# Kernel tuning notes

Measured on AMD Instinct MI355X. Metric: run time of the kernel, lower is better.

Reference implementation:

```python
import jax, jax.numpy as jnp
import numpy as np

K_EXPERTS = 2  # init kwarg k_experts

def _glu_mlp(x, up_w, gate_w, down_w):
    # gated MLP: down( up(x) * GELU(gate(x)) ), exact-erf GELU matching torch nn.GELU()
    h = (x @ up_w) * jax.nn.gelu(x @ gate_w, approximate=False)
    return h @ down_w

def setup_inputs() -> dict:
    key = jax.random.key(0)
    ks = jax.random.split(key, 8)
    B, S, D, I, E = 2, 2048, 1024, 512, 8
    sc = 0.02
    return {
        "x": jax.random.normal(ks[0], (B, S, D), jnp.float32),
        "gate_w": jax.random.normal(ks[1], (E, D), jnp.float32) * sc,
        "up_w": jax.random.normal(ks[2], (E, D, I), jnp.float32) * sc,
        "gproj_w": jax.random.normal(ks[3], (E, D, I), jnp.float32) * sc,
        "down_w": jax.random.normal(ks[4], (E, I, D), jnp.float32) * sc,
        "shared_up_w": jax.random.normal(ks[5], (D, I), jnp.float32) * sc,
        "shared_gate_w": jax.random.normal(ks[6], (D, I), jnp.float32) * sc,
        "shared_down_w": jax.random.normal(ks[7], (I, D), jnp.float32) * sc,
    }

def reference(x, gate_w, up_w, gproj_w, down_w, shared_up_w, shared_gate_w, shared_down_w):
    B, S, D = x.shape
    E = gate_w.shape[0]
    xf = x.reshape(-1, D)                      # [T, D]
    T = xf.shape[0]

    # --- SigmaGate: softmax over expert logits, top-k, renormalize ---
    logits = xf @ gate_w.T                     # [T, E]
    scores = jax.nn.softmax(logits, axis=-1)
    topk_w, topk_idx = jax.lax.top_k(scores, K_EXPERTS)   # [T, k]
    topk_w = topk_w / (topk_w.sum(axis=-1, keepdims=True) + 1e-20)

    # combine weights as dense [T, E] (topk indices are distinct per token)
    combine = jnp.zeros((T, E), xf.dtype).at[jnp.arange(T)[:, None], topk_idx].add(topk_w)

    # --- experts: scan over E, accumulate weighted expert outputs ---
    def step(acc, ws):
        uw, gw, dw, ce = ws                    # ce: [T] combine weight for this expert
        y_e = _glu_mlp(xf, uw, gw, dw)         # [T, D]
        return acc + ce[:, None] * y_e, None

    y, _ = jax.lax.scan(step, jnp.zeros_like(xf), (up_w, gproj_w, down_w, combine.T))

    # --- shared expert on identity ---
    y = y + _glu_mlp(xf, shared_up_w, shared_gate_w, shared_down_w)
    return y.reshape(B, S, D)
```

## Files before the change

kernel.cpp:

```cpp
#include <hip/hip_runtime.h>
#include <hip/hip_bf16.h>
#include <math.h>

#define T_TOK 4096
#define D_DIM 1024
#define I_DIM 512
#define E_EXP 8
#define KSEL 2
#define NPAIR (T_TOK * KSEL)
#define ROUTED_CAP 10240
#define SHARED_BASE ROUTED_CAP
#define RTOT (ROUTED_CAP + T_TOK)
#define MAXTILES 56
#define GRID_G (MAXTILES * 4)

typedef __bf16 bf16x8 __attribute__((ext_vector_type(8)));
typedef float f32x4 __attribute__((ext_vector_type(4)));
typedef unsigned short ushort8 __attribute__((ext_vector_type(8)));

constexpr size_t SZ_XB  = (size_t)T_TOK * D_DIM * 2;
constexpr size_t SZ_UG  = (size_t)E_EXP * 2 * I_DIM * D_DIM * 2;
constexpr size_t SZ_DT  = (size_t)E_EXP * I_DIM * D_DIM * 2;
constexpr size_t SZ_SUG = (size_t)2 * I_DIM * D_DIM * 2;
constexpr size_t SZ_SDT = (size_t)I_DIM * D_DIM * 2;
constexpr size_t SZ_H   = (size_t)RTOT * I_DIM * 2;
constexpr size_t SZ_Y   = (size_t)RTOT * D_DIM * 2;

constexpr size_t OFF_XB   = 0;
constexpr size_t OFF_UG   = OFF_XB  + SZ_XB;
constexpr size_t OFF_DT   = OFF_UG  + SZ_UG;
constexpr size_t OFF_SUG  = OFF_DT  + SZ_DT;
constexpr size_t OFF_SDT  = OFF_SUG + SZ_SUG;
constexpr size_t OFF_H    = OFF_SDT + SZ_SDT;
constexpr size_t OFF_Y    = OFF_H   + SZ_H;
constexpr size_t OFF_TOPKI= OFF_Y   + SZ_Y;
constexpr size_t OFF_TOPKW= OFF_TOPKI + (size_t)NPAIR * 4;
constexpr size_t OFF_INV  = OFF_TOPKW + (size_t)NPAIR * 4;
constexpr size_t OFF_PERM = OFF_INV   + (size_t)NPAIR * 4;
constexpr size_t OFF_META = OFF_PERM  + (size_t)RTOT * 4;

__device__ __forceinline__ unsigned short f2bf(float f) {
  unsigned int u = __float_as_uint(f);
  unsigned int r = (u + 0x7FFFu + ((u >> 16) & 1u)) >> 16;
  return (unsigned short)r;
}
__device__ __forceinline__ float bf2f(unsigned short s) {
  return __uint_as_float(((unsigned int)s) << 16);
}
__device__ __forceinline__ void gload_lds16(const void* g, void* l) {
  __builtin_amdgcn_global_load_lds(
      (const __attribute__((address_space(1))) void*)g,
      (__attribute__((address_space(3))) void*)l, 16, 0, 0);
}

__global__ void transpose_cvt_all(
    const float* __restrict__ upw, const float* __restrict__ gpw,
    const float* __restrict__ dww, const float* __restrict__ sup,
    const float* __restrict__ sgt, const float* __restrict__ sdw,
    unsigned short* __restrict__ UG, unsigned short* __restrict__ sUG,
    unsigned short* __restrict__ Dt, unsigned short* __restrict__ sDt) {
  __shared__ float t[32][33];
  int bid = blockIdx.x;
  const float* in; unsigned short* out;
  int R, C, xt, yt, mode;
  if (bid < 4096)       { int e = bid >> 9, s = bid & 511;
    in = upw + (size_t)e * D_DIM * I_DIM; out = UG + (size_t)e * 2 * I_DIM * D_DIM;
    R = D_DIM; C = I_DIM; xt = s & 15; yt = s >> 4; mode = 0; }
  else if (bid < 8192)  { int b = bid - 4096; int e = b >> 9, s = b & 511;
    in = gpw + (size_t)e * D_DIM * I_DIM; out = UG + (size_t)e * 2 * I_DIM * D_DIM;
    R = D_DIM; C = I_DIM; xt = s & 15; yt = s >> 4; mode = 1; }
  else if (bid < 12288) { int b = bid - 8192; int e = b >> 9, s = b & 511;
    in = dww + (size_t)e * I_DIM * D_DIM; out = Dt + (size_t)e * I_DIM * D_DIM;
    R = I_DIM; C = D_DIM; xt = s & 31; yt = s >> 5; mode = 2; }
  else if (bid < 12800) { int s = bid - 12288;
    in = sup; out = sUG; R = D_DIM; C = I_DIM; xt = s & 15; yt = s >> 4; mode = 0; }
  else if (bid < 13312) { int s = bid - 12800;
    in = sgt; out = sUG; R = D_DIM; C = I_DIM; xt = s & 15; yt = s >> 4; mode = 1; }
  else                  { int s = bid - 13312;
    in = sdw; out = sDt; R = I_DIM; C = D_DIM; xt = s & 31; yt = s >> 5; mode = 2; }
  int c0 = xt * 32, r0 = yt * 32;
  int tx = threadIdx.x, ty = threadIdx.y;
#pragma unroll
  for (int i = 0; i < 4; ++i)
    t[ty + 8 * i][tx] = in[(size_t)(r0 + ty + 8 * i) * C + c0 + tx];
  __syncthreads();
#pragma unroll
  for (int i = 0; i < 4; ++i) {
    int c = c0 + ty + 8 * i;
    int orow = (mode == 2) ? c : (((c >> 4) << 5) + (c & 15) + (mode == 1 ? 16 : 0));
    out[(size_t)orow * R + r0 + tx] = f2bf(t[tx][ty + 8 * i]);
  }
}

__global__ void gating_kernel(const float* __restrict__ x, const float* __restrict__ gw,
                              unsigned short* __restrict__ xb,
                              int* __restrict__ topk_idx, float* __restrict__ topk_w) {
  int lane = threadIdx.x & 63;
  int t = blockIdx.x * 4 + (threadIdx.x >> 6);
  const float4* xr = (const float4*)(x + (size_t)t * D_DIM);
  float4 xv[4];
#pragma unroll
  for (int j = 0; j < 4; ++j) xv[j] = xr[lane + 64 * j];
#pragma unroll
  for (int j = 0; j < 4; ++j) {
    ushort4 o;
    o.x = f2bf(xv[j].x); o.y = f2bf(xv[j].y); o.z = f2bf(xv[j].z); o.w = f2bf(xv[j].w);
    *(ushort4*)&xb[(size_t)t * D_DIM + (lane + 64 * j) * 4] = o;
  }
  float acc[E_EXP];
#pragma unroll
  for (int e = 0; e < E_EXP; ++e) {
    const float4* gr = (const float4*)(gw + (size_t)e * D_DIM);
    float a = 0.f;
#pragma unroll
    for (int j = 0; j < 4; ++j) {
      float4 g = gr[lane + 64 * j];
      a += xv[j].x * g.x + xv[j].y * g.y + xv[j].z * g.z + xv[j].w * g.w;
    }
    acc[e] = a;
  }
#pragma unroll
  for (int off = 32; off; off >>= 1)
#pragma unroll
    for (int e = 0; e < E_EXP; ++e) acc[e] += __shfl_xor(acc[e], off, 64);
  if (lane == 0) {
    int i0 = 0; float m0 = acc[0];
#pragma unroll
    for (int e = 1; e < E_EXP; ++e) if (acc[e] > m0) { m0 = acc[e]; i0 = e; }
    int i1 = -1; float m1 = -1e30f;
#pragma unroll
    for (int e = 0; e < E_EXP; ++e) if (e != i0 && acc[e] > m1) { m1 = acc[e]; i1 = e; }
    float e1 = __expf(m1 - m0);
    float w0 = 1.0f / (1.0f + e1);
    float w1 = e1 / (1.0f + e1);
    topk_idx[2 * t] = i0; topk_idx[2 * t + 1] = i1;
    topk_w[2 * t] = w0;   topk_w[2 * t + 1] = w1;
  }
}

__global__ __launch_bounds__(1024) void route_kernel(
    const int* __restrict__ tidx, int* __restrict__ meta,
    int* __restrict__ perm, int* __restrict__ inv) {
  __shared__ int els[NPAIR];
  __shared__ int cnt_iw[128][E_EXP];
  __shared__ int base_iw[128][E_EXP];
  __shared__ int ebase[E_EXP];
  __shared__ int ecnt[E_EXP];
  int tid = threadIdx.x, lane = tid & 63, wv = tid >> 6;

  for (int it = 0; it < NPAIR / 1024; ++it) {
    int g = it * 1024 + tid;
    int e = tidx[g];
    els[g] = e;
#pragma unroll
    for (int ex = 0; ex < E_EXP; ++ex) {
      unsigned long long m = __ballot(e == ex);
      if (lane == 0) cnt_iw[it * 16 + wv][ex] = __popcll(m);
    }
  }
  __syncthreads();

  if (tid < E_EXP) {
    int s = 0;
    for (int iw = 0; iw < 128; ++iw) { base_iw[iw][tid] = s; s += cnt_iw[iw][tid]; }
    ecnt[tid] = s;
  }
  __syncthreads();

  if (tid == 0) {
    int o = 0, tc = 0;
    int2* m2 = (int2*)meta;
    for (int e = 0; e < E_EXP; ++e) {
      ebase[e] = o;
      int c = ecnt[e];
      int pt = (c + 255) >> 8;
      for (int ti = 0; ti < pt; ++ti) m2[tc++] = make_int2(e, o + ti * 256);
      o += pt * 256;
    }
    for (int ti = 0; ti < T_TOK / 256; ++ti)
      m2[tc++] = make_int2(E_EXP, SHARED_BASE + ti * 256);
    for (; tc < MAXTILES; ++tc) m2[tc] = make_int2(-1, 0);
  }
  __syncthreads();

  for (int it = 0; it < NPAIR / 1024; ++it) {
    int g = it * 1024 + tid;
    int e = els[g];
    int rank = 0;
#pragma unroll
    for (int ex = 0; ex < E_EXP; ++ex) {
      unsigned long long m = __ballot(e == ex);
      if (e == ex) rank = __popcll(m & ((1ull << lane) - 1ull));
    }
    int row = ebase[e] + base_iw[it * 16 + wv][e] + rank;
    perm[row] = g >> 1;
    inv[g] = row;
  }
  for (int p = tid; p < E_EXP * 256; p += 1024) {
    int e = p >> 8, s = p & 255;
    int c = ecnt[e];
    int padn = (((c + 255) >> 8) << 8) - c;
    if (s < padn) perm[ebase[e] + c + s] = 0;
  }
  for (int t = tid; t < T_TOK; t += 1024) perm[SHARED_BASE + t] = t;
}

__global__ __launch_bounds__(512, 2) void gemm1_kernel(
    const unsigned short* __restrict__ xb, const unsigned short* __restrict__ UG,
    const unsigned short* __restrict__ sUG, unsigned short* __restrict__ H,
    const int* __restrict__ meta, const int* __restrict__ perm) {
  int orig = blockIdx.x;
  int wg = (orig & 7) * (GRID_G / 8) + (orig >> 3);
  int mt = wg >> 2, nt = wg & 3;
  int2 m2 = ((const int2*)meta)[mt];
  int e = m2.x;
  if (e < 0) return;
  int base = m2.y;
  int n0 = nt * 256;
  const unsigned short* B = (e < E_EXP) ? UG + (size_t)e * 2 * I_DIM * D_DIM : sUG;

  __shared__ unsigned short As[2 * 256 * 64];
  __shared__ unsigned short Bs[2 * 256 * 64];

  int tid = threadIdx.x, lane = tid & 63, wv = tid >> 6;
  const unsigned short *gA[4], *gB[4];
  int dL[4];
#pragma unroll
  for (int j = 0; j < 4; ++j) {
    int c = j * 512 + tid;
    int row = c >> 3, q = c & 7, qs = q ^ (row & 7);
    int tok = perm[base + row];
    gA[j] = xb + (size_t)tok * D_DIM + qs * 8;
    gB[j] = B + (size_t)(n0 + row) * D_DIM + qs * 8;
    dL[j] = (j * 512 + wv * 64) * 8;
  }

  f32x4 acc[8][4] = {};
  int wr = (wv >> 2) * 128, wc = (wv & 3) * 64;
  int l15 = lane & 15, l4 = lane >> 4;
  int sx = l15 & 7;

#define STAGE1(buf, k0) do { \
  _Pragma("unroll") \
  for (int j = 0; j < 4; ++j) { \
    gload_lds16(gA[j] + (k0), As + (buf) * 16384 + dL[j]); \
    gload_lds16(gB[j] + (k0), Bs + (buf) * 16384 + dL[j]); \
  } } while (0)

  STAGE1(0, 0);
  const int NK = D_DIM / 64;
  for (int t = 0; t < NK; ++t) {
    int cur = t & 1;
    if (t + 1 < NK) {
      STAGE1(cur ^ 1, (t + 1) * 64);
      asm volatile("s_waitcnt vmcnt(8)" ::: "memory");
    } else {
      asm volatile("s_waitcnt vmcnt(0)" ::: "memory");
    }
    __builtin_amdgcn_s_barrier();
#pragma unroll
    for (int kh = 0; kh < 2; ++kh) {
      int kb = kh * 4 + l4;
      bf16x8 af[8], bfr[4];
#pragma unroll
      for (int i = 0; i < 8; ++i)
        af[i] = *reinterpret_cast<const bf16x8*>(&As[cur * 16384 + (wr + i * 16 + l15) * 64 + (kb ^ sx) * 8]);
#pragma unroll
      for (int j = 0; j < 4; ++j)
        bfr[j] = *reinterpret_cast<const bf16x8*>(&Bs[cur * 16384 + (wc + j * 16 + l15) * 64 + (kb ^ sx) * 8]);
      __builtin_amdgcn_s_setprio(1);
#pragma unroll
      for (int i = 0; i < 8; ++i)
#pragma unroll
        for (int j = 0; j < 4; ++j)
          acc[i][j] = __builtin_amdgcn_mfma_f32_16x16x32_bf16(af[i], bfr[j], acc[i][j], 0, 0, 0);
      __builtin_amdgcn_s_setprio(0);
    }
    asm volatile("" ::: "memory");
    __builtin_amdgcn_s_barrier();
  }
#undef STAGE1

  const float is2 = 0.70710678118654752f;
  int cb = ((n0 + wc) >> 1);
#pragma unroll
  for (int i = 0; i < 8; ++i) {
    int row = base + wr + i * 16 + l4 * 4;
#pragma unroll
    for (int p = 0; p < 2; ++p) {
      int col = cb + p * 16 + l15;
#pragma unroll
      for (int r = 0; r < 4; ++r) {
        float u = acc[i][2 * p][r], g = acc[i][2 * p + 1][r];
        float gl = 0.5f * g * (1.0f + erff(g * is2));
        H[(size_t)(row + r) * I_DIM + col] = f2bf(u * gl);
      }
    }
  }
}

__global__ __launch_bounds__(512, 2) void gemm2_kernel(
    const unsigned short* __restrict__ H, const unsigned short* __restrict__ Dt,
    const unsigned short* __restrict__ sDt, unsigned short* __restrict__ Y,
    const int* __restrict__ meta) {
  int orig = blockIdx.x;
  int wg = (orig & 7) * (GRID_G / 8) + (orig >> 3);
  int mt = wg >> 2, nt = wg & 3;
  int2 m2 = ((const int2*)meta)[mt];
  int e = m2.x;
  if (e < 0) return;
  int base = m2.y;
  int n0 = nt * 256;
  const unsigned short* B = (e < E_EXP) ? Dt + (size_t)e * D_DIM * I_DIM : sDt;

  __shared__ unsigned short As[2 * 256 * 64];
  __shared__ unsigned short Bs[2 * 256 * 64];

  int tid = threadIdx.x, lane = tid & 63, wv = tid >> 6;
  const unsigned short *gA[4], *gB[4];
  int dL[4];
#pragma unroll
  for (int j = 0; j < 4; ++j) {
    int c = j * 512 + tid;
    int row = c >> 3, q = c & 7, qs = q ^ (row & 7);
    gA[j] = H + (size_t)(base + row) * I_DIM + qs * 8;
    gB[j] = B + (size_t)(n0 + row) * I_DIM + qs * 8;
    dL[j] = (j * 512 + wv * 64) * 8;
  }

  f32x4 acc[8][4] = {};
  int wr = (wv >> 2) * 128, wc = (wv & 3) * 64;
  int l15 = lane & 15, l4 = lane >> 4;
  int sx = l15 & 7;

#define STAGE2(buf, k0) do { \
  _Pragma("unroll") \
  for (int j = 0; j < 4; ++j) { \
    gload_lds16(gA[j] + (k0), As + (buf) * 16384 + dL[j]); \
    gload_lds16(gB[j] + (k0), Bs + (buf) * 16384 + dL[j]); \
  } } while (0)

  STAGE2(0, 0);
  const int NK = I_DIM / 64;
  for (int t = 0; t < NK; ++t) {
    int cur = t & 1;
    if (t + 1 < NK) {
      STAGE2(cur ^ 1, (t + 1) * 64);
      asm volatile("s_waitcnt vmcnt(8)" ::: "memory");
    } else {
      asm volatile("s_waitcnt vmcnt(0)" ::: "memory");
    }
    __builtin_amdgcn_s_barrier();
#pragma unroll
    for (int kh = 0; kh < 2; ++kh) {
      int kb = kh * 4 + l4;
      bf16x8 af[8], bfr[4];
#pragma unroll
      for (int i = 0; i < 8; ++i)
        af[i] = *reinterpret_cast<const bf16x8*>(&As[cur * 16384 + (wr + i * 16 + l15) * 64 + (kb ^ sx) * 8]);
#pragma unroll
      for (int j = 0; j < 4; ++j)
        bfr[j] = *reinterpret_cast<const bf16x8*>(&Bs[cur * 16384 + (wc + j * 16 + l15) * 64 + (kb ^ sx) * 8]);
      __builtin_amdgcn_s_setprio(1);
#pragma unroll
      for (int i = 0; i < 8; ++i)
#pragma unroll
        for (int j = 0; j < 4; ++j)
          acc[i][j] = __builtin_amdgcn_mfma_f32_16x16x32_bf16(af[i], bfr[j], acc[i][j], 0, 0, 0);
      __builtin_amdgcn_s_setprio(0);
    }
    asm volatile("" ::: "memory");
    __builtin_amdgcn_s_barrier();
  }
#undef STAGE2

#pragma unroll
  for (int i = 0; i < 8; ++i) {
    int row = base + wr + i * 16 + l4 * 4;
#pragma unroll
    for (int j = 0; j < 4; ++j) {
      int col = n0 + wc + j * 16 + l15;
#pragma unroll
      for (int r = 0; r < 4; ++r)
        Y[(size_t)(row + r) * D_DIM + col] = f2bf(acc[i][j][r]);
    }
  }
}

__global__ void combine_kernel(const unsigned short* __restrict__ Y, const int* __restrict__ inv,
                               const float* __restrict__ tw, float* __restrict__ out) {
  int g = blockIdx.x * 256 + threadIdx.x;
  int t = g >> 7, d0 = (g & 127) * 8;
  int r0 = inv[2 * t], r1 = inv[2 * t + 1];
  float w0 = tw[2 * t], w1 = tw[2 * t + 1];
  ushort8 y0 = *(const ushort8*)&Y[(size_t)r0 * D_DIM + d0];
  ushort8 y1 = *(const ushort8*)&Y[(size_t)r1 * D_DIM + d0];
  ushort8 ys = *(const ushort8*)&Y[(size_t)(SHARED_BASE + t) * D_DIM + d0];
  float o[8];
#pragma unroll
  for (int j = 0; j < 8; ++j)
    o[j] = w0 * bf2f(y0[j]) + w1 * bf2f(y1[j]) + bf2f(ys[j]);
  float4* op = (float4*)(out + (size_t)t * D_DIM + d0);
  op[0] = make_float4(o[0], o[1], o[2], o[3]);
  op[1] = make_float4(o[4], o[5], o[6], o[7]);
}

extern "C" void kernel_launch(void* const* d_in, const int* in_sizes, int n_in,
                              void* d_out, int out_size, void* d_ws, size_t ws_size,
                              hipStream_t stream) {
  const float* x    = (const float*)d_in[0];
  const float* gw   = (const float*)d_in[1];
  const float* upw  = (const float*)d_in[2];
  const float* gpw  = (const float*)d_in[3];
  const float* dww  = (const float*)d_in[4];
  const float* sup  = (const float*)d_in[5];
  const float* sgt  = (const float*)d_in[6];
  const float* sdw  = (const float*)d_in[7];
  float* out = (float*)d_out;

  char* ws = (char*)d_ws;
  unsigned short* xb  = (unsigned short*)(ws + OFF_XB);
  unsigned short* UG  = (unsigned short*)(ws + OFF_UG);
  unsigned short* Dt  = (unsigned short*)(ws + OFF_DT);
  unsigned short* sUG = (unsigned short*)(ws + OFF_SUG);
  unsigned short* sDt = (unsigned short*)(ws + OFF_SDT);
  unsigned short* H   = (unsigned short*)(ws + OFF_H);
  unsigned short* Y   = (unsigned short*)(ws + OFF_Y);
  int*   tki   = (int*)(ws + OFF_TOPKI);
  float* tkw   = (float*)(ws + OFF_TOPKW);
  int*   inv   = (int*)(ws + OFF_INV);
  int*   perm  = (int*)(ws + OFF_PERM);
  int*   meta  = (int*)(ws + OFF_META);

  transpose_cvt_all<<<13824, dim3(32, 8), 0, stream>>>(upw, gpw, dww, sup, sgt, sdw,
                                                       UG, sUG, Dt, sDt);
  gating_kernel<<<T_TOK / 4, 256, 0, stream>>>(x, gw, xb, tki, tkw);
  route_kernel<<<1, 1024, 0, stream>>>(tki, meta, perm, inv);

  gemm1_kernel<<<GRID_G, 512, 0, stream>>>(xb, UG, sUG, H, meta, perm);
  gemm2_kernel<<<GRID_G, 512, 0, stream>>>(H, Dt, sDt, Y, meta);
  combine_kernel<<<(T_TOK * 128) / 256, 256, 0, stream>>>(Y, inv, tkw, out);
}
```

Baseline: 110.6 us.

## Interleave next-tile global-to-LDS loads with MFMA sub-blocks in both GEMM kernels

Splits each K-step of the two expert GEMM kernels into four MFMA sub-blocks, each using half the A rows and half the K slice. The next tile's global-to-LDS loads are issued one chunk between each sub-block instead of all at once before compute. The trailing barrier moves to the loop top and the wait count drops to vmcnt(2). The aim is to hide load latency and shrink the fragment registers (af[4] instead of af[8]). Correctness depends on the earlier chunks' loads having landed before the barrier, which relies on in-order vmcnt semantics and the barrier placement. The added sched_barriers also constrain how the compiler can reorder instructions.

Result: slower. 116.5 us (+5.3%).

```diff
diff --git a/kernel.cpp b/kernel.cpp
--- a/kernel.cpp
+++ b/kernel.cpp
@@ -205,6 +205,7 @@
   for (int t = tid; t < T_TOK; t += 1024) perm[SHARED_BASE + t] = t;
 }
 
+
 __global__ __launch_bounds__(512, 2) void gemm1_kernel(
     const unsigned short* __restrict__ xb, const unsigned short* __restrict__ UG,
     const unsigned short* __restrict__ sUG, unsigned short* __restrict__ H,
@@ -240,46 +241,89 @@
   int l15 = lane & 15, l4 = lane >> 4;
   int sx = l15 & 7;
 
-#define STAGE1(buf, k0) do { \
-  _Pragma("unroll") \
-  for (int j = 0; j < 4; ++j) { \
+#define LOAD2_1(j, buf, k0) do { \
     gload_lds16(gA[j] + (k0), As + (buf) * 16384 + dL[j]); \
-    gload_lds16(gB[j] + (k0), Bs + (buf) * 16384 + dL[j]); \
-  } } while (0)
-
-  STAGE1(0, 0);
+    gload_lds16(gB[j] + (k0), Bs + (buf) * 16384 + dL[j]); } while (0)
+
+#pragma unroll
+  for (int j = 0; j < 4; ++j) LOAD2_1(j, 0, 0);
+
   const int NK = D_DIM / 64;
   for (int t = 0; t < NK; ++t) {
-    int cur = t & 1;
-    if (t + 1 < NK) {
-      STAGE1(cur ^ 1, (t + 1) * 64);
-      asm volatile("s_waitcnt vmcnt(8)" ::: "memory");
+    int cur = t & 1, nxt = cur ^ 1;
+    int kn = (t + 1) * 64;
+    bool pf = (t + 1 < NK);
+    __builtin_amdgcn_s_barrier();
+    if (pf) { LOAD2_1(0, nxt, kn);
+      asm volatile("s_waitcnt vmcnt(2)" ::: "memory");
     } else {
       asm volatile("s_waitcnt vmcnt(0)" ::: "memory");
     }
     __builtin_amdgcn_s_barrier();
-#pragma unroll
-    for (int kh = 0; kh < 2; ++kh) {
-      int kb = kh * 4 + l4;
-      bf16x8 af[8], bfr[4];
-#pragma unroll
-      for (int i = 0; i < 8; ++i)
-        af[i] = *reinterpret_cast<const bf16x8*>(&As[cur * 16384 + (wr + i * 16 + l15) * 64 + (kb ^ sx) * 8]);
-#pragma unroll
-      for (int j = 0; j < 4; ++j)
-        bfr[j] = *reinterpret_cast<const bf16x8*>(&Bs[cur * 16384 + (wc + j * 16 + l15) * 64 + (kb ^ sx) * 8]);
-      __builtin_amdgcn_s_setprio(1);
-#pragma unroll
-      for (int i = 0; i < 8; ++i)
+    bf16x8 af[4], bfr[4];
+    const unsigned short* Ac = As + cur * 16384;
+    const unsigned short* Bc = Bs + cur * 16384;
+    {
+      int kb = (0 + l4) ^ sx;
+#pragma unroll
+      for (int j = 0; j < 4; ++j) bfr[j] = *(const bf16x8*)&Bc[(wc + j * 16 + l15) * 64 + kb * 8];
+#pragma unroll
+      for (int i = 0; i < 4; ++i) af[i] = *(const bf16x8*)&Ac[(wr + i * 16 + l15) * 64 + kb * 8];
+      __builtin_amdgcn_s_setprio(1);
+#pragma unroll
+      for (int i = 0; i < 4; ++i)
 #pragma unroll
         for (int j = 0; j < 4; ++j)
           acc[i][j] = __builtin_amdgcn_mfma_f32_16x16x32_bf16(af[i], bfr[j], acc[i][j], 0, 0, 0);
       __builtin_amdgcn_s_setprio(0);
-    }
-    asm volatile("" ::: "memory");
-    __builtin_amdgcn_s_barrier();
-  }
-#undef STAGE1
+      __builtin_amdgcn_sched_barrier(0);
+    }
+    if (pf) LOAD2_1(1, nxt, kn);
+    {
+      int kb = (0 + l4) ^ sx;
+#pragma unroll
+      for (int i = 0; i < 4; ++i) af[i] = *(const bf16x8*)&Ac[(wr + (4 + i) * 16 + l15) * 64 + kb * 8];
+      __builtin_amdgcn_s_setprio(1);
+#pragma unroll
+      for (int i = 0; i < 4; ++i)
+#pragma unroll
+        for (int j = 0; j < 4; ++j)
+          acc[4 + i][j] = __builtin_amdgcn_mfma_f32_16x16x32_bf16(af[i], bfr[j], acc[4 + i][j], 0, 0, 0);
+      __builtin_amdgcn_s_setprio(0);
+      __builtin_amdgcn_sched_barrier(0);
+    }
+    if (pf) LOAD2_1(2, nxt, kn);
+    {
+      int kb = (4 + l4) ^ sx;
+#pragma unroll
+      for (int j = 0; j < 4; ++j) bfr[j] = *(const bf16x8*)&Bc[(wc + j * 16 + l15) * 64 + kb * 8];
+#pragma unroll
+      for (int i = 0; i < 4; ++i) af[i] = *(const bf16x8*)&Ac[(wr + i * 16 + l15) * 64 + kb * 8];
+      __builtin_amdgcn_s_setprio(1);
+#pragma unroll
+      for (int i = 0; i < 4; ++i)
+#pragma unroll
+        for (int j = 0; j < 4; ++j)
+          acc[i][j] = __builtin_amdgcn_mfma_f32_16x16x32_bf16(af[i], bfr[j], acc[i][j], 0, 0, 0);
+      __builtin_amdgcn_s_setprio(0);
+      __builtin_amdgcn_sched_barrier(0);
+    }
+    if (pf) LOAD2_1(3, nxt, kn);
+    {
+      int kb = (4 + l4) ^ sx;
+#pragma unroll
+      for (int i = 0; i < 4; ++i) af[i] = *(const bf16x8*)&Ac[(wr + (4 + i) * 16 + l15) * 64 + kb * 8];
+      __builtin_amdgcn_s_setprio(1);
+#pragma unroll
+      for (int i = 0; i < 4; ++i)
+#pragma unroll
+        for (int j = 0; j < 4; ++j)
+          acc[4 + i][j] = __builtin_amdgcn_mfma_f32_16x16x32_bf16(af[i], bfr[j], acc[4 + i][j], 0, 0, 0);
+      __builtin_amdgcn_s_setprio(0);
+      __builtin_amdgcn_sched_barrier(0);
+    }
+  }
+#undef LOAD2_1
 
   const float is2 = 0.70710678118654752f;
   int cb = ((n0 + wc) >> 1);
@@ -333,46 +377,89 @@
   int l15 = lane & 15, l4 = lane >> 4;
   int sx = l15 & 7;
 
-#define STAGE2(buf, k0) do { \
-  _Pragma("unroll") \
-  for (int j = 0; j < 4; ++j) { \
+#define LOAD2_2(j, buf, k0) do { \
     gload_lds16(gA[j] + (k0), As + (buf) * 16384 + dL[j]); \
-    gload_lds16(gB[j] + (k0), Bs + (buf) * 16384 + dL[j]); \
-  } } while (0)
-
-  STAGE2(0, 0);
+    gload_lds16(gB[j] + (k0), Bs + (buf) * 16384 + dL[j]); } while (0)
+
+#pragma unroll
+  for (int j = 0; j < 4; ++j) LOAD2_2(j, 0, 0);
+
   const int NK = I_DIM / 64;
   for (int t = 0; t < NK; ++t) {
-    int cur = t & 1;
-    if (t + 1 < NK) {
-      STAGE2(cur ^ 1, (t + 1) * 64);
-      asm volatile("s_waitcnt vmcnt(8)" ::: "memory");
+    int cur = t & 1, nxt = cur ^ 1;
+    int kn = (t + 1) * 64;
+    bool pf = (t + 1 < NK);
+    __builtin_amdgcn_s_barrier();
+    if (pf) { LOAD2_2(0, nxt, kn);
+      asm volatile("s_waitcnt vmcnt(2)" ::: "memory");
     } else {
       asm volatile("s_waitcnt vmcnt(0)" ::: "memory");
     }
     __builtin_amdgcn_s_barrier();
-#pragma unroll
-    for (int kh = 0; kh < 2; ++kh) {
-      int kb = kh * 4 + l4;
-      bf16x8 af[8], bfr[4];
-#pragma unroll
-      for (int i = 0; i < 8; ++i)
-        af[i] = *reinterpret_cast<const bf16x8*>(&As[cur * 16384 + (wr + i * 16 + l15) * 64 + (kb ^ sx) * 8]);
-#pragma unroll
-      for (int j = 0; j < 4; ++j)
-        bfr[j] = *reinterpret_cast<const bf16x8*>(&Bs[cur * 16384 + (wc + j * 16 + l15) * 64 + (kb ^ sx) * 8]);
-      __builtin_amdgcn_s_setprio(1);
-#pragma unroll
-      for (int i = 0; i < 8; ++i)
+    bf16x8 af[4], bfr[4];
+    const unsigned short* Ac = As + cur * 16384;
+    const unsigned short* Bc = Bs + cur * 16384;
+    {
+      int kb = (0 + l4) ^ sx;
+#pragma unroll
+      for (int j = 0; j < 4; ++j) bfr[j] = *(const bf16x8*)&Bc[(wc + j * 16 + l15) * 64 + kb * 8];
+#pragma unroll
+      for (int i = 0; i < 4; ++i) af[i] = *(const bf16x8*)&Ac[(wr + i * 16 + l15) * 64 + kb * 8];
+      __builtin_amdgcn_s_setprio(1);
+#pragma unroll
+      for (int i = 0; i < 4; ++i)
 #pragma unroll
         for (int j = 0; j < 4; ++j)
           acc[i][j] = __builtin_amdgcn_mfma_f32_16x16x32_bf16(af[i], bfr[j], acc[i][j], 0, 0, 0);
       __builtin_amdgcn_s_setprio(0);
-    }
-    asm volatile("" ::: "memory");
-    __builtin_amdgcn_s_barrier();
-  }
-#undef STAGE2
+      __builtin_amdgcn_sched_barrier(0);
+    }
+    if (pf) LOAD2_2(1, nxt, kn);
+    {
+      int kb = (0 + l4) ^ sx;
+#pragma unroll
+      for (int i = 0; i < 4; ++i) af[i] = *(const bf16x8*)&Ac[(wr + (4 + i) * 16 + l15) * 64 + kb * 8];
+      __builtin_amdgcn_s_setprio(1);
+#pragma unroll
+      for (int i = 0; i < 4; ++i)
+#pragma unroll
+        for (int j = 0; j < 4; ++j)
+          acc[4 + i][j] = __builtin_amdgcn_mfma_f32_16x16x32_bf16(af[i], bfr[j], acc[4 + i][j], 0, 0, 0);
+      __builtin_amdgcn_s_setprio(0);
+      __builtin_amdgcn_sched_barrier(0);
+    }
+    if (pf) LOAD2_2(2, nxt, kn);
+    {
+      int kb = (4 + l4) ^ sx;
+#pragma unroll
+      for (int j = 0; j < 4; ++j) bfr[j] = *(const bf16x8*)&Bc[(wc + j * 16 + l15) * 64 + kb * 8];
+#pragma unroll
+      for (int i = 0; i < 4; ++i) af[i] = *(const bf16x8*)&Ac[(wr + i * 16 + l15) * 64 + kb * 8];
+      __builtin_amdgcn_s_setprio(1);
+#pragma unroll
+      for (int i = 0; i < 4; ++i)
+#pragma unroll
+        for (int j = 0; j < 4; ++j)
+          acc[i][j] = __builtin_amdgcn_mfma_f32_16x16x32_bf16(af[i], bfr[j], acc[i][j], 0, 0, 0);
+      __builtin_amdgcn_s_setprio(0);
+      __builtin_amdgcn_sched_barrier(0);
+    }
+    if (pf) LOAD2_2(3, nxt, kn);
+    {
+      int kb = (4 + l4) ^ sx;
+#pragma unroll
+      for (int i = 0; i < 4; ++i) af[i] = *(const bf16x8*)&Ac[(wr + (4 + i) * 16 + l15) * 64 + kb * 8];
+      __builtin_amdgcn_s_setprio(1);
+#pragma unroll
+      for (int i = 0; i < 4; ++i)
+#pragma unroll
+        for (int j = 0; j < 4; ++j)
+          acc[4 + i][j] = __builtin_amdgcn_mfma_f32_16x16x32_bf16(af[i], bfr[j], acc[4 + i][j], 0, 0, 0);
+      __builtin_amdgcn_s_setprio(0);
+      __builtin_amdgcn_sched_barrier(0);
+    }
+  }
+#undef LOAD2_2
 
 #pragma unroll
   for (int i = 0; i < 8; ++i) {
```

## Fuse transpose and gating kernels; interleave prefetch with MFMA quarters in gemm1

Applied to the files above, without the earlier changes.

Merges the weight transpose/convert kernel and the gating kernel into one launch, with block index selecting the role, to save a launch and let the two overlap. Restructures the gemm1 main loop into four MFMA quarters, each preceded by a slice of the next tile's global-to-LDS prefetch, with explicit lgkmcnt waits and scheduling barriers. This spreads memory traffic across the compute phase at the cost of more barriers per K step. gemm2 only gets cosmetic cast changes.

Result: slower. 124.1 us (+12.2%).

```diff
diff --git a/kernel.cpp b/kernel.cpp
--- a/kernel.cpp
+++ b/kernel.cpp
@@ -13,6 +13,7 @@
 #define RTOT (ROUTED_CAP + T_TOK)
 #define MAXTILES 56
 #define GRID_G (MAXTILES * 4)
+#define NTRB 13824
 
 typedef __bf16 bf16x8 __attribute__((ext_vector_type(8)));
 typedef float f32x4 __attribute__((ext_vector_type(4)));
@@ -53,88 +54,90 @@
       (__attribute__((address_space(3))) void*)l, 16, 0, 0);
 }
 
-__global__ void transpose_cvt_all(
+__global__ __launch_bounds__(256) void prep_kernel(
+    const float* __restrict__ x,   const float* __restrict__ gw,
     const float* __restrict__ upw, const float* __restrict__ gpw,
     const float* __restrict__ dww, const float* __restrict__ sup,
     const float* __restrict__ sgt, const float* __restrict__ sdw,
     unsigned short* __restrict__ UG, unsigned short* __restrict__ sUG,
-    unsigned short* __restrict__ Dt, unsigned short* __restrict__ sDt) {
-  __shared__ float t[32][33];
+    unsigned short* __restrict__ Dt, unsigned short* __restrict__ sDt,
+    unsigned short* __restrict__ xb,
+    int* __restrict__ topk_idx, float* __restrict__ topk_w) {
+  __shared__ float tbuf[32][33];
   int bid = blockIdx.x;
-  const float* in; unsigned short* out;
-  int R, C, xt, yt, mode;
-  if (bid < 4096)       { int e = bid >> 9, s = bid & 511;
-    in = upw + (size_t)e * D_DIM * I_DIM; out = UG + (size_t)e * 2 * I_DIM * D_DIM;
-    R = D_DIM; C = I_DIM; xt = s & 15; yt = s >> 4; mode = 0; }
-  else if (bid < 8192)  { int b = bid - 4096; int e = b >> 9, s = b & 511;
-    in = gpw + (size_t)e * D_DIM * I_DIM; out = UG + (size_t)e * 2 * I_DIM * D_DIM;
-    R = D_DIM; C = I_DIM; xt = s & 15; yt = s >> 4; mode = 1; }
-  else if (bid < 12288) { int b = bid - 8192; int e = b >> 9, s = b & 511;
-    in = dww + (size_t)e * I_DIM * D_DIM; out = Dt + (size_t)e * I_DIM * D_DIM;
-    R = I_DIM; C = D_DIM; xt = s & 31; yt = s >> 5; mode = 2; }
-  else if (bid < 12800) { int s = bid - 12288;
-    in = sup; out = sUG; R = D_DIM; C = I_DIM; xt = s & 15; yt = s >> 4; mode = 0; }
-  else if (bid < 13312) { int s = bid - 12800;
-    in = sgt; out = sUG; R = D_DIM; C = I_DIM; xt = s & 15; yt = s >> 4; mode = 1; }
-  else                  { int s = bid - 13312;
-    in = sdw; out = sDt; R = I_DIM; C = D_DIM; xt = s & 31; yt = s >> 5; mode = 2; }
-  int c0 = xt * 32, r0 = yt * 32;
-  int tx = threadIdx.x, ty = threadIdx.y;
-#pragma unroll
-  for (int i = 0; i < 4; ++i)
-    t[ty + 8 * i][tx] = in[(size_t)(r0 + ty + 8 * i) * C + c0 + tx];
-  __syncthreads();
-#pragma unroll
-  for (int i = 0; i < 4; ++i) {
-    int c = c0 + ty + 8 * i;
-    int orow = (mode == 2) ? c : (((c >> 4) << 5) + (c & 15) + (mode == 1 ? 16 : 0));
-    out[(size_t)orow * R + r0 + tx] = f2bf(t[tx][ty + 8 * i]);
-  }
-}
-
-__global__ void gating_kernel(const float* __restrict__ x, const float* __restrict__ gw,
-                              unsigned short* __restrict__ xb,
-                              int* __restrict__ topk_idx, float* __restrict__ topk_w) {
-  int lane = threadIdx.x & 63;
-  int t = blockIdx.x * 4 + (threadIdx.x >> 6);
-  const float4* xr = (const float4*)(x + (size_t)t * D_DIM);
-  float4 xv[4];
-#pragma unroll
-  for (int j = 0; j < 4; ++j) xv[j] = xr[lane + 64 * j];
-#pragma unroll
-  for (int j = 0; j < 4; ++j) {
-    ushort4 o;
-    o.x = f2bf(xv[j].x); o.y = f2bf(xv[j].y); o.z = f2bf(xv[j].z); o.w = f2bf(xv[j].w);
-    *(ushort4*)&xb[(size_t)t * D_DIM + (lane + 64 * j) * 4] = o;
-  }
-  float acc[E_EXP];
-#pragma unroll
-  for (int e = 0; e < E_EXP; ++e) {
-    const float4* gr = (const float4*)(gw + (size_t)e * D_DIM);
-    float a = 0.f;
+  int tid = threadIdx.x;
+  if (bid < NTRB) {
+    const float* in; unsigned short* out;
+    int R, C, xt, yt, mode;
+    if (bid < 4096)       { int e = bid >> 9, s = bid & 511;
+      in = upw + (size_t)e * D_DIM * I_DIM; out = UG + (size_t)e * 2 * I_DIM * D_DIM;
+      R = D_DIM; C = I_DIM; xt = s & 15; yt = s >> 4; mode = 0; }
+    else if (bid < 8192)  { int b = bid - 4096; int e = b >> 9, s = b & 511;
+      in = gpw + (size_t)e * D_DIM * I_DIM; out = UG + (size_t)e * 2 * I_DIM * D_DIM;
+      R = D_DIM; C = I_DIM; xt = s & 15; yt = s >> 4; mode = 1; }
+    else if (bid < 12288) { int b = bid - 8192; int e = b >> 9, s = b & 511;
+      in = dww + (size_t)e * I_DIM * D_DIM; out = Dt + (size_t)e * I_DIM * D_DIM;
+      R = I_DIM; C = D_DIM; xt = s & 31; yt = s >> 5; mode = 2; }
+    else if (bid < 12800) { int s = bid - 12288;
+      in = sup; out = sUG; R = D_DIM; C = I_DIM; xt = s & 15; yt = s >> 4; mode = 0; }
+    else if (bid < 13312) { int s = bid - 12800;
+      in = sgt; out = sUG; R = D_DIM; C = I_DIM; xt = s & 15; yt = s >> 4; mode = 1; }
+    else                  { int s = bid - 13312;
+      in = sdw; out = sDt; R = I_DIM; C = D_DIM; xt = s & 31; yt = s >> 5; mode = 2; }
+    int c0 = xt * 32, r0 = yt * 32;
+    int tx = tid & 31, ty = tid >> 5;
+#pragma unroll
+    for (int i = 0; i < 4; ++i)
+      tbuf[ty + 8 * i][tx] = in[(size_t)(r0 + ty + 8 * i) * C + c0 + tx];
+    __syncthreads();
+#pragma unroll
+    for (int i = 0; i < 4; ++i) {
+      int c = c0 + ty + 8 * i;
+      int orow = (mode == 2) ? c : (((c >> 4) << 5) + (c & 15) + (mode == 1 ? 16 : 0));
+      out[(size_t)orow * R + r0 + tx] = f2bf(tbuf[tx][ty + 8 * i]);
+    }
+  } else {
+    int lane = tid & 63;
+    int t = (bid - NTRB) * 4 + (tid >> 6);
+    const float4* xr = (const float4*)(x + (size_t)t * D_DIM);
+    float4 xv[4];
+#pragma unroll
+    for (int j = 0; j < 4; ++j) xv[j] = xr[lane + 64 * j];
 #pragma unroll
     for (int j = 0; j < 4; ++j) {
-      float4 g = gr[lane + 64 * j];
-      a += xv[j].x * g.x + xv[j].y * g.y + xv[j].z * g.z + xv[j].w * g.w;
-    }
-    acc[e] = a;
-  }
-#pragma unroll
-  for (int off = 32; off; off >>= 1)
-#pragma unroll
-    for (int e = 0; e < E_EXP; ++e) acc[e] += __shfl_xor(acc[e], off, 64);
-  if (lane == 0) {
-    int i0 = 0; float m0 = acc[0];
-#pragma unroll
-    for (int e = 1; e < E_EXP; ++e) if (acc[e] > m0) { m0 = acc[e]; i0 = e; }
-    int i1 = -1; float m1 = -1e30f;
-#pragma unroll
-    for (int e = 0; e < E_EXP; ++e) if (e != i0 && acc[e] > m1) { m1 = acc[e]; i1 = e; }
-    float e1 = __expf(m1 - m0);
-    float w0 = 1.0f / (1.0f + e1);
-    float w1 = e1 / (1.0f + e1);
-    topk_idx[2 * t] = i0; topk_idx[2 * t + 1] = i1;
-    topk_w[2 * t] = w0;   topk_w[2 * t + 1] = w1;
+      ushort4 o;
+      o.x = f2bf(xv[j].x); o.y = f2bf(xv[j].y); o.z = f2bf(xv[j].z); o.w = f2bf(xv[j].w);
+      *(ushort4*)&xb[(size_t)t * D_DIM + (lane + 64 * j) * 4] = o;
+    }
+    float acc[E_EXP];
+#pragma unroll
+    for (int e = 0; e < E_EXP; ++e) {
+      const float4* gr = (const float4*)(gw + (size_t)e * D_DIM);
+      float a = 0.f;
+#pragma unroll
+      for (int j = 0; j < 4; ++j) {
+        float4 g = gr[lane + 64 * j];
+        a += xv[j].x * g.x + xv[j].y * g.y + xv[j].z * g.z + xv[j].w * g.w;
+      }
+      acc[e] = a;
+    }
+#pragma unroll
+    for (int off = 32; off; off >>= 1)
+#pragma unroll
+      for (int e = 0; e < E_EXP; ++e) acc[e] += __shfl_xor(acc[e], off, 64);
+    if (lane == 0) {
+      int i0 = 0; float m0 = acc[0];
+#pragma unroll
+      for (int e = 1; e < E_EXP; ++e) if (acc[e] > m0) { m0 = acc[e]; i0 = e; }
+      int i1 = -1; float m1 = -1e30f;
+#pragma unroll
+      for (int e = 0; e < E_EXP; ++e) if (e != i0 && acc[e] > m1) { m1 = acc[e]; i1 = e; }
+      float e1 = __expf(m1 - m0);
+      float w0 = 1.0f / (1.0f + e1);
+      float w1 = e1 / (1.0f + e1);
+      topk_idx[2 * t] = i0; topk_idx[2 * t + 1] = i1;
+      topk_w[2 * t] = w0;   topk_w[2 * t + 1] = w1;
+    }
   }
 }
 
@@ -240,46 +243,72 @@
   int l15 = lane & 15, l4 = lane >> 4;
   int sx = l15 & 7;
 
-#define STAGE1(buf, k0) do { \
-  _Pragma("unroll") \
-  for (int j = 0; j < 4; ++j) { \
+#define LOAD2_1(j, buf, k0) do { \
     gload_lds16(gA[j] + (k0), As + (buf) * 16384 + dL[j]); \
-    gload_lds16(gB[j] + (k0), Bs + (buf) * 16384 + dL[j]); \
-  } } while (0)
-
-  STAGE1(0, 0);
+    gload_lds16(gB[j] + (k0), Bs + (buf) * 16384 + dL[j]); } while (0)
+
+#define MFMA16(lo) do { \
+    __builtin_amdgcn_s_setprio(1); \
+    _Pragma("unroll") \
+    for (int i = 0; i < 4; ++i) \
+      _Pragma("unroll") \
+      for (int j = 0; j < 4; ++j) \
+        acc[(lo) + i][j] = __builtin_amdgcn_mfma_f32_16x16x32_bf16(af[i], bfr[j], acc[(lo) + i][j], 0, 0, 0); \
+    __builtin_amdgcn_s_setprio(0); } while (0)
+
+#pragma unroll
+  for (int j = 0; j < 4; ++j) LOAD2_1(j, 0, 0);
+
   const int NK = D_DIM / 64;
   for (int t = 0; t < NK; ++t) {
-    int cur = t & 1;
-    if (t + 1 < NK) {
-      STAGE1(cur ^ 1, (t + 1) * 64);
-      asm volatile("s_waitcnt vmcnt(8)" ::: "memory");
+    int cur = t & 1, nxt = cur ^ 1;
+    int kn = (t + 1) * 64;
+    bool pf = (t + 1 < NK);
+    const unsigned short* Ac = As + cur * 16384;
+    const unsigned short* Bc = Bs + cur * 16384;
+    bf16x8 af[4], bfr[4];
+    int kb0 = l4 ^ sx, kb1 = (4 + l4) ^ sx;
+
+    if (pf) { LOAD2_1(0, nxt, kn);
+      asm volatile("s_waitcnt vmcnt(2)" ::: "memory");
     } else {
       asm volatile("s_waitcnt vmcnt(0)" ::: "memory");
     }
     __builtin_amdgcn_s_barrier();
 #pragma unroll
-    for (int kh = 0; kh < 2; ++kh) {
-      int kb = kh * 4 + l4;
-      bf16x8 af[8], bfr[4];
-#pragma unroll
-      for (int i = 0; i < 8; ++i)
-        af[i] = *reinterpret_cast<const bf16x8*>(&As[cur * 16384 + (wr + i * 16 + l15) * 64 + (kb ^ sx) * 8]);
-#pragma unroll
-      for (int j = 0; j < 4; ++j)
-        bfr[j] = *reinterpret_cast<const bf16x8*>(&Bs[cur * 16384 + (wc + j * 16 + l15) * 64 + (kb ^ sx) * 8]);
-      __builtin_amdgcn_s_setprio(1);
-#pragma unroll
-      for (int i = 0; i < 8; ++i)
-#pragma unroll
-        for (int j = 0; j < 4; ++j)
-          acc[i][j] = __builtin_amdgcn_mfma_f32_16x16x32_bf16(af[i], bfr[j], acc[i][j], 0, 0, 0);
-      __builtin_amdgcn_s_setprio(0);
-    }
-    asm volatile("" ::: "memory");
-    __builtin_amdgcn_s_barrier();
-  }
-#undef STAGE1
+    for (int j = 0; j < 4; ++j) bfr[j] = *(const bf16x8*)&Bc[(wc + j * 16 + l15) * 64 + kb0 * 8];
+#pragma unroll
+    for (int i = 0; i < 4; ++i) af[i] = *(const bf16x8*)&Ac[(wr + i * 16 + l15) * 64 + kb0 * 8];
+    asm volatile("s_waitcnt lgkmcnt(0)" ::: "memory");
+    __builtin_amdgcn_sched_barrier(0);
+    MFMA16(0);
+    __builtin_amdgcn_s_barrier();
+    if (pf) LOAD2_1(1, nxt, kn);
+#pragma unroll
+    for (int i = 0; i < 4; ++i) af[i] = *(const bf16x8*)&Ac[(wr + (4 + i) * 16 + l15) * 64 + kb0 * 8];
+    asm volatile("s_waitcnt lgkmcnt(0)" ::: "memory");
+    __builtin_amdgcn_sched_barrier(0);
+    MFMA16(4);
+    __builtin_amdgcn_s_barrier();
+    if (pf) LOAD2_1(2, nxt, kn);
+#pragma unroll
+    for (int j = 0; j < 4; ++j) bfr[j] = *(const bf16x8*)&Bc[(wc + j * 16 + l15) * 64 + kb1 * 8];
+#pragma unroll
+    for (int i = 0; i < 4; ++i) af[i] = *(const bf16x8*)&Ac[(wr + i * 16 + l15) * 64 + kb1 * 8];
+    asm volatile("s_waitcnt lgkmcnt(0)" ::: "memory");
+    __builtin_amdgcn_sched_barrier(0);
+    MFMA16(0);
+    __builtin_amdgcn_s_barrier();
+    if (pf) LOAD2_1(3, nxt, kn);
+#pragma unroll
+    for (int i = 0; i < 4; ++i) af[i] = *(const bf16x8*)&Ac[(wr + (4 + i) * 16 + l15) * 64 + kb1 * 8];
+    asm volatile("s_waitcnt lgkmcnt(0)" ::: "memory");
+    __builtin_amdgcn_sched_barrier(0);
+    MFMA16(4);
+    __builtin_amdgcn_s_barrier();
+  }
+#undef LOAD2_1
+#undef MFMA16
 
   const float is2 = 0.70710678118654752f;
   int cb = ((n0 + wc) >> 1);
@@ -357,10 +386,10 @@
       bf16x8 af[8], bfr[4];
 #pragma unroll
       for (int i = 0; i < 8; ++i)
-        af[i] = *reinterpret_cast<const bf16x8*>(&As[cur * 16384 + (wr + i * 16 + l15) * 64 + (kb ^ sx) * 8]);
+        af[i] = *(const bf16x8*)&As[cur * 16384 + (wr + i * 16 + l15) * 64 + ((kb ^ sx)) * 8];
 #pragma unroll
       for (int j = 0; j < 4; ++j)
-        bfr[j] = *reinterpret_cast<const bf16x8*>(&Bs[cur * 16384 + (wc + j * 16 + l15) * 64 + (kb ^ sx) * 8]);
+        bfr[j] = *(const bf16x8*)&Bs[cur * 16384 + (wc + j * 16 + l15) * 64 + ((kb ^ sx)) * 8];
       __builtin_amdgcn_s_setprio(1);
 #pragma unroll
       for (int i = 0; i < 8; ++i)
@@ -432,9 +461,8 @@
   int*   perm  = (int*)(ws + OFF_PERM);
   int*   meta  = (int*)(ws + OFF_META);
 
-  transpose_cvt_all<<<13824, dim3(32, 8), 0, stream>>>(upw, gpw, dww, sup, sgt, sdw,
-                                                       UG, sUG, Dt, sDt);
-  gating_kernel<<<T_TOK / 4, 256, 0, stream>>>(x, gw, xb, tki, tkw);
+  prep_kernel<<<NTRB + T_TOK / 4, 256, 0, stream>>>(x, gw, upw, gpw, dww, sup, sgt, sdw,
+                                                    UG, sUG, Dt, sDt, xb, tki, tkw);
   route_kernel<<<1, 1024, 0, stream>>>(tki, meta, perm, inv);
 
   gemm1_kernel<<<GRID_G, 512, 0, stream>>>(xb, UG, sUG, H, meta, perm);
```

## Switch gemm1 to four-stage BK=32 LDS pipeline with one barrier per step

Applied to the files above, without the earlier changes.

The gate/up GEMM kernel drops its double-buffered K=64 tiles for a 4-slot ring of K=32 tiles. Three stages are prefetched ahead, with graded vmcnt waits and a single barrier per iteration. The XOR swizzle is adjusted to the 4-chunk row width. The aim is to hide global-to-LDS latency behind deeper prefetch and to cut one barrier per step, at the cost of twice as many loop iterations and fewer MFMAs per barrier.

New measurement: 118.7 us. +7.3%, slower.

```diff
diff --git a/kernel.cpp b/kernel.cpp
--- a/kernel.cpp
+++ b/kernel.cpp
@@ -219,16 +219,16 @@
   int n0 = nt * 256;
   const unsigned short* B = (e < E_EXP) ? UG + (size_t)e * 2 * I_DIM * D_DIM : sUG;
 
-  __shared__ unsigned short As[2 * 256 * 64];
-  __shared__ unsigned short Bs[2 * 256 * 64];
+  __shared__ unsigned short As[4 * 256 * 32];
+  __shared__ unsigned short Bs[4 * 256 * 32];
 
   int tid = threadIdx.x, lane = tid & 63, wv = tid >> 6;
-  const unsigned short *gA[4], *gB[4];
-  int dL[4];
-#pragma unroll
-  for (int j = 0; j < 4; ++j) {
+  const unsigned short *gA[2], *gB[2];
+  int dL[2];
+#pragma unroll
+  for (int j = 0; j < 2; ++j) {
     int c = j * 512 + tid;
-    int row = c >> 3, q = c & 7, qs = q ^ (row & 7);
+    int row = c >> 2, q = c & 3, qs = q ^ (row & 3);
     int tok = perm[base + row];
     gA[j] = xb + (size_t)tok * D_DIM + qs * 8;
     gB[j] = B + (size_t)(n0 + row) * D_DIM + qs * 8;
@@ -238,48 +238,47 @@
   f32x4 acc[8][4] = {};
   int wr = (wv >> 2) * 128, wc = (wv & 3) * 64;
   int l15 = lane & 15, l4 = lane >> 4;
-  int sx = l15 & 7;
-
-#define STAGE1(buf, k0) do { \
+  int sx = l15 & 3;
+
+#define STG1(bufi, k0) do { \
   _Pragma("unroll") \
-  for (int j = 0; j < 4; ++j) { \
-    gload_lds16(gA[j] + (k0), As + (buf) * 16384 + dL[j]); \
-    gload_lds16(gB[j] + (k0), Bs + (buf) * 16384 + dL[j]); \
+  for (int j = 0; j < 2; ++j) { \
+    gload_lds16(gA[j] + (k0), As + (bufi) * 8192 + dL[j]); \
+    gload_lds16(gB[j] + (k0), Bs + (bufi) * 8192 + dL[j]); \
   } } while (0)
 
-  STAGE1(0, 0);
-  const int NK = D_DIM / 64;
+  STG1(0, 0); STG1(1, 32); STG1(2, 64);
+
+  const int NK = D_DIM / 32;
   for (int t = 0; t < NK; ++t) {
-    int cur = t & 1;
-    if (t + 1 < NK) {
-      STAGE1(cur ^ 1, (t + 1) * 64);
-      asm volatile("s_waitcnt vmcnt(8)" ::: "memory");
-    } else {
-      asm volatile("s_waitcnt vmcnt(0)" ::: "memory");
-    }
+    int p = t & 3;
+    if (t < NK - 2)      asm volatile("s_waitcnt vmcnt(8)" ::: "memory");
+    else if (t < NK - 1) asm volatile("s_waitcnt vmcnt(4)" ::: "memory");
+    else                 asm volatile("s_waitcnt vmcnt(0)" ::: "memory");
     __builtin_amdgcn_s_barrier();
-#pragma unroll
-    for (int kh = 0; kh < 2; ++kh) {
-      int kb = kh * 4 + l4;
-      bf16x8 af[8], bfr[4];
-#pragma unroll
-      for (int i = 0; i < 8; ++i)
-        af[i] = *reinterpret_cast<const bf16x8*>(&As[cur * 16384 + (wr + i * 16 + l15) * 64 + (kb ^ sx) * 8]);
+    if (t + 3 < NK) STG1((t + 3) & 3, (t + 3) * 32);
+    const unsigned short* Ac = As + p * 8192;
+    const unsigned short* Bc = Bs + p * 8192;
+    bf16x8 af[8], bfr[4];
+#pragma unroll
+    for (int i = 0; i < 8; ++i) {
+      int row = wr + i * 16 + l15;
+      af[i] = *(const bf16x8*)&Ac[row * 32 + (l4 ^ sx) * 8];
+    }
+#pragma unroll
+    for (int j = 0; j < 4; ++j) {
+      int row = wc + j * 16 + l15;
+      bfr[j] = *(const bf16x8*)&Bc[row * 32 + (l4 ^ sx) * 8];
+    }
+    __builtin_amdgcn_s_setprio(1);
+#pragma unroll
+    for (int i = 0; i < 8; ++i)
 #pragma unroll
       for (int j = 0; j < 4; ++j)
-        bfr[j] = *reinterpret_cast<const bf16x8*>(&Bs[cur * 16384 + (wc + j * 16 + l15) * 64 + (kb ^ sx) * 8]);
-      __builtin_amdgcn_s_setprio(1);
-#pragma unroll
-      for (int i = 0; i < 8; ++i)
-#pragma unroll
-        for (int j = 0; j < 4; ++j)
-          acc[i][j] = __builtin_amdgcn_mfma_f32_16x16x32_bf16(af[i], bfr[j], acc[i][j], 0, 0, 0);
-      __builtin_amdgcn_s_setprio(0);
-    }
-    asm volatile("" ::: "memory");
-    __builtin_amdgcn_s_barrier();
-  }
-#undef STAGE1
+        acc[i][j] = __builtin_amdgcn_mfma_f32_16x16x32_bf16(af[i], bfr[j], acc[i][j], 0, 0, 0);
+    __builtin_amdgcn_s_setprio(0);
+  }
+#undef STG1
 
   const float is2 = 0.70710678118654752f;
   int cb = ((n0 + wc) >> 1);
@@ -357,10 +356,10 @@
       bf16x8 af[8], bfr[4];
 #pragma unroll
       for (int i = 0; i < 8; ++i)
-        af[i] = *reinterpret_cast<const bf16x8*>(&As[cur * 16384 + (wr + i * 16 + l15) * 64 + (kb ^ sx) * 8]);
+        af[i] = *(const bf16x8*)&As[cur * 16384 + (wr + i * 16 + l15) * 64 + ((kb ^ sx)) * 8];
 #pragma unroll
       for (int j = 0; j < 4; ++j)
-        bfr[j] = *reinterpret_cast<const bf16x8*>(&Bs[cur * 16384 + (wc + j * 16 + l15) * 64 + (kb ^ sx) * 8]);
+        bfr[j] = *(const bf16x8*)&Bs[cur * 16384 + (wc + j * 16 + l15) * 64 + ((kb ^ sx)) * 8];
       __builtin_amdgcn_s_setprio(1);
 #pragma unroll
       for (int i = 0; i < 8; ++i)
```
